# Performance work log

Measured on AMD Instinct MI355X. Metric: run time of the kernel, lower is better.

Reference implementation:

```python
import jax, jax.numpy as jnp
import numpy as np

# Dimensions (source globals scaled to production: r=256 residues, s=128 sequences)
S, R, CM, CZ, C, H = 128, 256, 256, 128, 32, 8
EPS = 1e-5  # torch LayerNorm default


def setup_inputs() -> dict:
    key = jax.random.key(0)
    ks = jax.random.split(key, 14)
    msa = jax.random.normal(ks[0], (S, R, CM), dtype=jnp.float32)
    pair = jax.random.normal(ks[1], (R, R, CZ), dtype=jnp.float32)
    u = lambda k, shape, fan: jax.random.uniform(k, shape, jnp.float32, -1.0 / np.sqrt(fan), 1.0 / np.sqrt(fan))
    return {
        "msa": msa,
        "pair": pair,
        # per-head LayerNorm affine params (stacked over head axis)
        "ln_msa_g": 1.0 + 0.1 * jax.random.normal(ks[2], (H, CM), dtype=jnp.float32),
        "ln_msa_b": 0.1 * jax.random.normal(ks[3], (H, CM), dtype=jnp.float32),
        "ln_pair_g": 1.0 + 0.1 * jax.random.normal(ks[4], (H, CZ), dtype=jnp.float32),
        "ln_pair_b": 0.1 * jax.random.normal(ks[5], (H, CZ), dtype=jnp.float32),
        # per-head projections (torch Linear without bias; stored as (in, out))
        "Wq": u(ks[6], (H, CM, C), CM),
        "Wk": u(ks[7], (H, CM, C), CM),
        "Wv": u(ks[8], (H, CM, C), CM),
        "Wg": u(ks[9], (H, CM, C), CM),
        "Wb": u(ks[10], (H, CZ, S), CZ),  # linear_b: c_z -> s
        # output projection c*H -> c_m (with bias)
        "Wo": u(ks[11], (H * C, CM), H * C),
        "bo": u(ks[12], (CM,), H * C),
    }


def _forward(msa, pair, ln_msa_g, ln_msa_b, ln_pair_g, ln_pair_b, Wq, Wk, Wv, Wg, Wb, Wo, bo):
    # LayerNorm normalization is head-independent; only affine differs per head.
    mu = msa.mean(-1, keepdims=True)
    var = msa.var(-1, keepdims=True)
    nm = (msa - mu) * jax.lax.rsqrt(var + EPS)              # (S, R, CM)
    p = nm[None] * ln_msa_g[:, None, None, :] + ln_msa_b[:, None, None, :]  # (H, S, R, CM)

    q = jnp.einsum("hsrc,hcd->hsrd", p, Wq)                  # (H, S, R, C)
    k = jnp.einsum("hsrc,hcd->hsrd", p, Wk)
    v = jnp.einsum("hsrc,hcd->hsrd", p, Wv)
    g = jax.nn.sigmoid(jnp.einsum("hsrc,hcd->hsrd", p, Wg))

    pmu = pair.mean(-1, keepdims=True)
    pvar = pair.var(-1, keepdims=True)
    npair = (pair - pmu) * jax.lax.rsqrt(pvar + EPS)         # (R, R, CZ)
    pp = npair[None] * ln_pair_g[:, None, None, :] + ln_pair_b[:, None, None, :]  # (H, R, R, CZ)
    bflat = jnp.einsum("hijc,hcs->hijs", pp, Wb)             # (H, R, R, S)
    # Faithful to torch: b = linear_b(flat_pair).view(s, r, r) -- a raw
    # row-major reinterpretation (NOT a transpose).
    b = bflat.reshape(H, S, R, R)

    inv_sqrt_c = np.float32(1.0 / np.sqrt(C))
    scores = (jnp.einsum("hsid,hsjd->hsij", q, k) + b) * inv_sqrt_c  # (H, S, R, R)
    # Source softmax is over dim=-2 (the query/row axis), faithful here.
    a = jax.nn.softmax(scores, axis=-2)
    o = g * jnp.einsum("hsij,hsjd->hsid", a, v)              # (H, S, R, C)

    # concat heads on last dim: (S, R, H*C)
    cat = jnp.transpose(o, (1, 2, 0, 3)).reshape(S, R, H * C)
    return cat @ Wo + bo                                      # (S, R, CM)


def reference(msa, pair, ln_msa_g, ln_msa_b, ln_pair_g, ln_pair_b, Wq, Wk, Wv, Wg, Wb, Wo, bo):
    return _forward(msa, pair, ln_msa_g, ln_msa_b, ln_pair_g, ln_pair_b, Wq, Wk, Wv, Wg, Wb, Wo, bo)
```

## Files before the change

### kernel.cpp

```cpp
#include <hip/hip_runtime.h>
#include <hip/hip_bf16.h>


namespace {
constexpr int S_ = 128, R_ = 256, CM_ = 256, CZ_ = 128, C_ = 32, H_ = 8;
constexpr int SR_ = S_ * R_;
constexpr int RR_ = R_ * R_;
constexpr float EPS_ = 1e-5f;
constexpr float ISC_ = 0.17677669529663687f;

constexpr size_t OFF_WC  = 0;
constexpr size_t OFF_BC  = 131072;
constexpr size_t OFF_BBP = 132096;
constexpr size_t F32_END = 133120;
constexpr size_t BF_BASE = F32_END * 4;
constexpr size_t QKVG_ELEMS  = (size_t)H_ * SR_ * C_;
constexpr size_t CAT_ELEMS   = (size_t)SR_ * CM_;
constexpr size_t WBT_ELEMS   = (size_t)H_ * 128 * 128;
constexpr size_t WOT_ELEMS   = (size_t)256 * 256;
constexpr size_t PAIRN_ELEMS = (size_t)RR_ * 128;
constexpr size_t MSAN_ELEMS  = (size_t)SR_ * 256;
constexpr size_t NEED_BYTES =
    BF_BASE +
    (4 * QKVG_ELEMS + CAT_ELEMS + WBT_ELEMS + WOT_ELEMS + PAIRN_ELEMS + MSAN_ELEMS) * 2;
}

typedef unsigned short bf_t;
typedef short s8v __attribute__((ext_vector_type(8)));
typedef float f4v __attribute__((ext_vector_type(4)));

__device__ __forceinline__ unsigned pk2(float lo, float hi) {
  __hip_bfloat162 t = __float22bfloat162_rn(float2{lo, hi});
  return *reinterpret_cast<unsigned*>(&t);
}
__device__ __forceinline__ bf_t pk1(float v) {
  __hip_bfloat16 t = __float2bfloat16(v);
  return *reinterpret_cast<bf_t*>(&t);
}
__device__ __forceinline__ float uplo(unsigned u) { return __uint_as_float(u << 16); }
__device__ __forceinline__ f4v mfma16(s8v a, s8v b, f4v c) {
  return __builtin_amdgcn_mfma_f32_16x16x32_bf16(a, b, c, 0, 0, 0);
}
__device__ __forceinline__ s8v ld8(const bf_t* p) { return *reinterpret_cast<const s8v*>(p); }

__global__ __launch_bounds__(512) void norm_all_k(const float* __restrict__ pair,
                                                  const float* __restrict__ msa,
                                                  bf_t* __restrict__ pairN,
                                                  bf_t* __restrict__ msaN) {
  int b = blockIdx.x;
  int lane = threadIdx.x & 63;
  if (b < RR_ / 8) {
    int row = b * 8 + (threadIdx.x >> 6);
    float2 v = reinterpret_cast<const float2*>(pair + (size_t)row * CZ_)[lane];
    float s = v.x + v.y;
    float s2 = v.x * v.x + v.y * v.y;
    for (int off = 32; off; off >>= 1) {
      s += __shfl_xor(s, off);
      s2 += __shfl_xor(s2, off);
    }
    float m = s / CZ_;
    float rs = rsqrtf(s2 / CZ_ - m * m + EPS_);
    reinterpret_cast<unsigned*>(pairN)[(size_t)row * 64 + lane] =
        pk2((v.x - m) * rs, (v.y - m) * rs);
  } else {
    int row = (b - RR_ / 8) * 8 + (threadIdx.x >> 6);
    float4 v = reinterpret_cast<const float4*>(msa + (size_t)row * CM_)[lane];
    float s = v.x + v.y + v.z + v.w;
    float s2 = v.x * v.x + v.y * v.y + v.z * v.z + v.w * v.w;
    for (int off = 32; off; off >>= 1) {
      s += __shfl_xor(s, off);
      s2 += __shfl_xor(s2, off);
    }
    float m = s / CM_;
    float rs = rsqrtf(s2 / CM_ - m * m + EPS_);
    uint2 wv;
    wv.x = pk2((v.x - m) * rs, (v.y - m) * rs);
    wv.y = pk2((v.z - m) * rs, (v.w - m) * rs);
    reinterpret_cast<uint2*>(msaN)[(size_t)row * 64 + lane] = wv;
  }
}

__global__ void prep_small_k(const float* __restrict__ lnb_m, const float* __restrict__ lnb_p,
                             const float* __restrict__ Wq, const float* __restrict__ Wk,
                             const float* __restrict__ Wv, const float* __restrict__ Wg,
                             const float* __restrict__ Wb, float* __restrict__ bc,
                             float* __restrict__ bbp) {
  int b = blockIdx.x;
  int t = threadIdx.x;
  if (b < H_) {
    int h = b;
    int m = t >> 5, d = t & 31;
    const float* Wsrc = (m == 0) ? Wq : (m == 1) ? Wk : (m == 2) ? Wv : Wg;
    float scale = (m == 0) ? ISC_ : 1.0f;
    float bias = 0.f;
    for (int c = 0; c < CM_; c++) bias += lnb_m[h * CM_ + c] * Wsrc[((size_t)h * CM_ + c) * C_ + d];
    bc[h * 128 + t] = bias * scale;
  } else {
    int h = b - H_;
    float bias = 0.f;
    for (int c = 0; c < CZ_; c++) bias += lnb_p[h * CZ_ + c] * Wb[((size_t)h * CZ_ + c) * S_ + t];
    bbp[h * 128 + t] = bias * ISC_;
  }
}

__global__ __launch_bounds__(256) void prep_wide_k(
    const float* __restrict__ lng_m, const float* __restrict__ lng_p,
    const float* __restrict__ Wq, const float* __restrict__ Wk, const float* __restrict__ Wv,
    const float* __restrict__ Wg, const float* __restrict__ Wb, const float* __restrict__ Wo,
    bf_t* __restrict__ wct, bf_t* __restrict__ wbt, bf_t* __restrict__ wot) {
  int idx = blockIdx.x * 256 + threadIdx.x;
  if (idx < 262144) {
    int h = idx >> 15, rem = idx & 32767;
    int j = rem >> 8, c = rem & 255;
    int m = j >> 5, d = j & 31;
    const float* Wsrc = (m == 0) ? Wq : (m == 1) ? Wk : (m == 2) ? Wv : Wg;
    float scale = (m == 0) ? ISC_ : 1.0f;
    wct[idx] = pk1(lng_m[h * CM_ + c] * Wsrc[((size_t)h * CM_ + c) * C_ + d] * scale);
  } else if (idx < 262144 + 131072) {
    int i2 = idx - 262144;
    int h = i2 >> 14, rem = i2 & 16383;
    int t = rem >> 7, c = rem & 127;
    wbt[i2] = pk1(lng_p[h * CZ_ + c] * Wb[((size_t)h * CZ_ + c) * S_ + t] * ISC_);
  } else {
    int i3 = idx - 262144 - 131072;
    int n = i3 >> 8, k = i3 & 255;
    wot[i3] = pk1(Wo[(size_t)k * 256 + n]);
  }
}

__global__ __launch_bounds__(512, 1) void qkvg_mfma_k(
    const bf_t* __restrict__ msaN, const bf_t* __restrict__ wct, const float* __restrict__ bc,
    bf_t* __restrict__ q, bf_t* __restrict__ k, bf_t* __restrict__ v, bf_t* __restrict__ g) {
  __shared__ bf_t sm_a[128 * 256];
  __shared__ bf_t sm_w[128 * 256];
  int ib = blockIdx.x;
  int tid = threadIdx.x;
  int w = tid >> 6, l = tid & 63;
  int l15 = l & 15, l4 = l >> 4;
  int iw = w >> 2, jw = w & 3;
  int sr0 = ib * 128;
  int sx7 = l15 & 7;
#pragma unroll
  for (int rep = 0; rep < 8; rep++) {
    int flat = rep * 512 + tid;
    int row = flat >> 5, c = flat & 31;
    *reinterpret_cast<uint4*>(&sm_a[row * 256 + ((c ^ (row & 7)) << 3)]) =
        *reinterpret_cast<const uint4*>(msaN + (size_t)(sr0 + row) * 256 + c * 8);
  }
  for (int h = 0; h < H_; h++) {
    __syncthreads();
#pragma unroll
    for (int rep = 0; rep < 8; rep++) {
      int flat = rep * 512 + tid;
      int row = flat >> 5, c = flat & 31;
      *reinterpret_cast<uint4*>(&sm_w[row * 256 + ((c ^ (row & 7)) << 3)]) =
          *reinterpret_cast<const uint4*>(wct + ((size_t)h * 128 + row) * 256 + c * 8);
    }
    f4v acc[4][2];
#pragma unroll
    for (int jt = 0; jt < 2; jt++) {
      float bb = bc[h * 128 + jw * 32 + jt * 16 + l15];
#pragma unroll
      for (int it = 0; it < 4; it++) acc[it][jt] = f4v{bb, bb, bb, bb};
    }
    __syncthreads();
#pragma unroll
    for (int ks = 0; ks < 8; ks++) {
      int ch = ks * 4 + l4;
      s8v a[4], b[2];
#pragma unroll
      for (int it = 0; it < 4; it++)
        a[it] = ld8(&sm_a[(iw * 64 + it * 16 + l15) * 256 + ((ch ^ sx7) << 3)]);
#pragma unroll
      for (int jt = 0; jt < 2; jt++)
        b[jt] = ld8(&sm_w[(jw * 32 + jt * 16 + l15) * 256 + ((ch ^ sx7) << 3)]);
#pragma unroll
      for (int it = 0; it < 4; it++)
#pragma unroll
        for (int jt = 0; jt < 2; jt++) acc[it][jt] = mfma16(a[it], b[jt], acc[it][jt]);
    }
#pragma unroll
    for (int it = 0; it < 4; it++) {
#pragma unroll
      for (int jt = 0; jt < 2; jt++) {
        int j = jw * 32 + jt * 16 + l15;
        int m_ = j >> 5, d = j & 31;
        bf_t* dst = (m_ == 0) ? q : (m_ == 1) ? k : (m_ == 2) ? v : g;
#pragma unroll
        for (int r = 0; r < 4; r++) {
          int i = iw * 64 + it * 16 + l4 * 4 + r;
          float val = acc[it][jt][r];
          if (m_ == 3) val = 1.f / (1.f + __expf(-val));
          dst[((size_t)h * SR_ + sr0 + i) * C_ + d] = pk1(val);
        }
      }
    }
  }
}

__global__ __launch_bounds__(512, 1) void attn_mfma_k(
    const bf_t* __restrict__ pairN, const bf_t* __restrict__ wbt,
    const float* __restrict__ bbp, const bf_t* __restrict__ qg, const bf_t* __restrict__ kg,
    const bf_t* __restrict__ vg, const bf_t* __restrict__ gg, bf_t* __restrict__ cat) {
  __shared__ bf_t sm_pN[256 * 128];
  __shared__ bf_t sm_wt[64 * 128];
  __shared__ bf_t sm_p[256 * 64];
  __shared__ bf_t sm_q[256 * 40];
  __shared__ bf_t sm_k[64 * 40];
  __shared__ bf_t sm_vt[32 * 64];
  __shared__ float sm_redm[4 * 64];
  __shared__ float sm_reds[4 * 64];

  int b = blockIdx.x;
  int x = b & 7, t = b >> 3;
  int round = t >> 5, inner = t & 31;
  int sl = inner >> 3, h = inner & 7;
  int s = (round * 8 + x) * 4 + sl;

  int tid = threadIdx.x;
  int w = tid >> 6, l = tid & 63;
  int l15 = l & 15, l4 = l >> 4;
  int iw = w >> 1, jw = w & 1;
  int iw2 = w >> 1, dw = w & 1;
  size_t base = ((size_t)h * SR_ + (size_t)s * R_) * C_;

#pragma unroll
  for (int rep = 0; rep < 2; rep++) {
    int flat = rep * 512 + tid;
    int row = flat >> 2, c = flat & 3;
    *reinterpret_cast<uint4*>(&sm_q[row * 40 + c * 8]) =
        *reinterpret_cast<const uint4*>(qg + base + (size_t)row * C_ + c * 8);
  }

  f4v accO[4];
#pragma unroll
  for (int it = 0; it < 4; it++) accO[it] = f4v{0.f, 0.f, 0.f, 0.f};

  for (int p = 0; p < 2; p++) {
    __syncthreads();
#pragma unroll
    for (int rep = 0; rep < 8; rep++) {
      int flat = rep * 512 + tid;
      int row = flat >> 4, c = flat & 15;
      int gr = (2 * s + (row >> 7)) * 256 + 2 * (row & 127) + p;
      *reinterpret_cast<uint4*>(&sm_pN[row * 128 + ((c ^ (row & 7)) << 3)]) =
          *reinterpret_cast<const uint4*>(pairN + (size_t)gr * 128 + c * 8);
    }
    for (int jh = 0; jh < 2; jh++) {
      int j0 = p * 128 + jh * 64;
      __syncthreads();
#pragma unroll
      for (int rep = 0; rep < 2; rep++) {
        int flat = rep * 512 + tid;
        int row = flat >> 4, c = flat & 15;
        *reinterpret_cast<uint4*>(&sm_wt[row * 128 + ((c ^ (row & 7)) << 3)]) =
            *reinterpret_cast<const uint4*>(wbt + ((size_t)h * 128 + jh * 64 + row) * 128 +
                                            c * 8);
      }
      if (tid < 256) {
        int row = tid >> 2, c = tid & 3;
        *reinterpret_cast<uint4*>(&sm_k[row * 40 + c * 8]) =
            *reinterpret_cast<const uint4*>(kg + base + (size_t)(j0 + row) * C_ + c * 8);
      } else {
        int t2 = tid - 256;
        int j = t2 >> 2, dc = t2 & 3;
        uint4 u = *reinterpret_cast<const uint4*>(vg + base + (size_t)(j0 + j) * C_ + dc * 8);
        unsigned uu[4] = {u.x, u.y, u.z, u.w};
#pragma unroll
        for (int e = 0; e < 8; e++) {
          int d = dc * 8 + e;
          bf_t val = (bf_t)((uu[e >> 1] >> ((e & 1) * 16)) & 0xffff);
          sm_vt[d * 64 + ((((j >> 3) ^ (d & 7)) << 3) + (j & 7))] = val;
        }
      }
      f4v acc[4][2];
      {
        float bb0 = bbp[h * 128 + jh * 64 + jw * 32 + l15];
        float bb1 = bbp[h * 128 + jh * 64 + jw * 32 + 16 + l15];
#pragma unroll
        for (int it = 0; it < 4; it++) {
          acc[it][0] = f4v{bb0, bb0, bb0, bb0};
          acc[it][1] = f4v{bb1, bb1, bb1, bb1};
        }
      }
      __syncthreads();
      int sx7 = l15 & 7;
#pragma unroll
      for (int ks = 0; ks < 4; ks++) {
        int ch = (ks * 4 + l4);
        s8v a[4], b2[2];
#pragma unroll
        for (int it = 0; it < 4; it++)
          a[it] = ld8(&sm_pN[(iw * 64 + it * 16 + l15) * 128 + ((ch ^ sx7) << 3)]);
#pragma unroll
        for (int u = 0; u < 2; u++)
          b2[u] = ld8(&sm_wt[(jw * 32 + u * 16 + l15) * 128 + ((ch ^ sx7) << 3)]);
#pragma unroll
        for (int it = 0; it < 4; it++) {
          acc[it][0] = mfma16(a[it], b2[0], acc[it][0]);
          acc[it][1] = mfma16(a[it], b2[1], acc[it][1]);
        }
      }
      {
        s8v qa[4], kb[2];
#pragma unroll
        for (int it = 0; it < 4; it++)
          qa[it] = ld8(&sm_q[(iw * 64 + it * 16 + l15) * 40 + l4 * 8]);
#pragma unroll
        for (int u = 0; u < 2; u++)
          kb[u] = ld8(&sm_k[(jw * 32 + u * 16 + l15) * 40 + l4 * 8]);
#pragma unroll
        for (int it = 0; it < 4; it++) {
          acc[it][0] = mfma16(qa[it], kb[0], acc[it][0]);
          acc[it][1] = mfma16(qa[it], kb[1], acc[it][1]);
        }
      }
      float fac[2], mloc[2];
#pragma unroll
      for (int u = 0; u < 2; u++) {
        float m0 = -1e30f;
#pragma unroll
        for (int it = 0; it < 4; it++)
#pragma unroll
          for (int r = 0; r < 4; r++) m0 = fmaxf(m0, acc[it][u][r]);
        m0 = fmaxf(m0, __shfl_xor(m0, 16));
        m0 = fmaxf(m0, __shfl_xor(m0, 32));
        float s0 = 0.f;
#pragma unroll
        for (int it = 0; it < 4; it++)
#pragma unroll
          for (int r = 0; r < 4; r++) {
            float e = __expf(acc[it][u][r] - m0);
            acc[it][u][r] = e;
            s0 += e;
          }
        s0 += __shfl_xor(s0, 16);
        s0 += __shfl_xor(s0, 32);
        mloc[u] = m0;
        if (l < 16) {
          sm_redm[iw * 64 + jw * 32 + u * 16 + l] = m0;
          sm_reds[iw * 64 + jw * 32 + u * 16 + l] = s0;
        }
      }
      __syncthreads();
#pragma unroll
      for (int u = 0; u < 2; u++) {
        int jc = jw * 32 + u * 16 + l15;
        float M = fmaxf(fmaxf(sm_redm[jc], sm_redm[64 + jc]),
                        fmaxf(sm_redm[128 + jc], sm_redm[192 + jc]));
        float tot = 0.f;
#pragma unroll
        for (int gx = 0; gx < 4; gx++)
          tot += sm_reds[gx * 64 + jc] * __expf(sm_redm[gx * 64 + jc] - M);
        fac[u] = __expf(mloc[u] - M) / tot;
#pragma unroll
        for (int it = 0; it < 4; it++)
#pragma unroll
          for (int r = 0; r < 4; r++) {
            int i = iw * 64 + it * 16 + l4 * 4 + r;
            sm_p[i * 64 + ((((jc >> 3) ^ (i & 7)) << 3) + (jc & 7))] =
                pk1(acc[it][u][r] * fac[u]);
          }
      }
      __syncthreads();
#pragma unroll
      for (int ks = 0; ks < 2; ks++) {
        int ch = ks * 4 + l4;
        s8v vb = ld8(&sm_vt[(dw * 16 + l15) * 64 + ((ch ^ sx7) << 3)]);
#pragma unroll
        for (int it = 0; it < 4; it++) {
          s8v pa = ld8(&sm_p[(iw2 * 64 + it * 16 + l15) * 64 + ((ch ^ sx7) << 3)]);
          accO[it] = mfma16(pa, vb, accO[it]);
        }
      }
    }
  }
#pragma unroll
  for (int it = 0; it < 4; it++) {
#pragma unroll
    for (int r = 0; r < 4; r++) {
      int i = iw2 * 64 + it * 16 + l4 * 4 + r;
      int d = dw * 16 + l15;
      float gf = uplo((unsigned)gg[base + (size_t)i * C_ + d]);
      cat[((size_t)s * R_ + i) * 256 + h * 32 + d] = pk1(accO[it][r] * gf);
    }
  }
}

__global__ __launch_bounds__(512, 1) void out_mfma_k(const bf_t* __restrict__ cat,
                                                     const bf_t* __restrict__ wot,
                                                     const float* __restrict__ bo,
                                                     float* __restrict__ out) {
  __shared__ bf_t sm_a[128 * 256];
  __shared__ bf_t sm_b[128 * 256];
  int ib = blockIdx.x;
  int tid = threadIdx.x;
  int w = tid >> 6, l = tid & 63;
  int l15 = l & 15, l4 = l >> 4, sx7 = l15 & 7;
  int iw = w >> 2, jw = w & 3;
  int sr0 = ib * 128;
#pragma unroll
  for (int rep = 0; rep < 8; rep++) {
    int flat = rep * 512 + tid;
    int row = flat >> 5, c = flat & 31;
    *reinterpret_cast<uint4*>(&sm_a[row * 256 + ((c ^ (row & 7)) << 3)]) =
        *reinterpret_cast<const uint4*>(cat + (size_t)(sr0 + row) * 256 + c * 8);
  }
  for (int nb = 0; nb < 2; nb++) {
    __syncthreads();
#pragma unroll
    for (int rep = 0; rep < 8; rep++) {
      int flat = rep * 512 + tid;
      int row = flat >> 5, c = flat & 31;
      *reinterpret_cast<uint4*>(&sm_b[row * 256 + ((c ^ (row & 7)) << 3)]) =
          *reinterpret_cast<const uint4*>(wot + (size_t)(nb * 128 + row) * 256 + c * 8);
    }
    f4v acc[4][2];
#pragma unroll
    for (int jt = 0; jt < 2; jt++) {
      float bb = bo[nb * 128 + jw * 32 + jt * 16 + l15];
#pragma unroll
      for (int it = 0; it < 4; it++) acc[it][jt] = f4v{bb, bb, bb, bb};
    }
    __syncthreads();
#pragma unroll
    for (int ks = 0; ks < 8; ks++) {
      int ch = ks * 4 + l4;
      s8v a[4], b[2];
#pragma unroll
      for (int it = 0; it < 4; it++)
        a[it] = ld8(&sm_a[(iw * 64 + it * 16 + l15) * 256 + ((ch ^ sx7) << 3)]);
#pragma unroll
      for (int jt = 0; jt < 2; jt++)
        b[jt] = ld8(&sm_b[(jw * 32 + jt * 16 + l15) * 256 + ((ch ^ sx7) << 3)]);
#pragma unroll
      for (int it = 0; it < 4; it++)
#pragma unroll
        for (int jt = 0; jt < 2; jt++) acc[it][jt] = mfma16(a[it], b[jt], acc[it][jt]);
    }
#pragma unroll
    for (int it = 0; it < 4; it++)
#pragma unroll
      for (int jt = 0; jt < 2; jt++) {
        int n = nb * 128 + jw * 32 + jt * 16 + l15;
#pragma unroll
        for (int r = 0; r < 4; r++) {
          int i = iw * 64 + it * 16 + l4 * 4 + r;
          out[(size_t)(sr0 + i) * 256 + n] = acc[it][jt][r];
        }
      }
  }
}

extern "C" void kernel_launch(void* const* d_in, const int* in_sizes, int n_in, void* d_out,
                              int out_size, void* d_ws, size_t ws_size, hipStream_t stream) {
  if (ws_size < NEED_BYTES) return;

  const float* msa = (const float*)d_in[0];
  const float* pair = (const float*)d_in[1];
  const float* lng_m = (const float*)d_in[2];
  const float* lnb_m = (const float*)d_in[3];
  const float* lng_p = (const float*)d_in[4];
  const float* lnb_p = (const float*)d_in[5];
  const float* Wq = (const float*)d_in[6];
  const float* Wk = (const float*)d_in[7];
  const float* Wv = (const float*)d_in[8];
  const float* Wg = (const float*)d_in[9];
  const float* Wb = (const float*)d_in[10];
  const float* Wo = (const float*)d_in[11];
  const float* bo = (const float*)d_in[12];
  float* out = (float*)d_out;
  float* ws = (float*)d_ws;

  bf_t* wct = (bf_t*)(ws + OFF_WC);
  float* bc = ws + OFF_BC;
  float* bbp = ws + OFF_BBP;
  bf_t* qb = (bf_t*)((char*)d_ws + BF_BASE);
  bf_t* kb = qb + QKVG_ELEMS;
  bf_t* vb = kb + QKVG_ELEMS;
  bf_t* gb = vb + QKVG_ELEMS;
  bf_t* cat = gb + QKVG_ELEMS;
  bf_t* wbt = cat + CAT_ELEMS;
  bf_t* wot = wbt + WBT_ELEMS;
  bf_t* pairN = wot + WOT_ELEMS;
  bf_t* msaN = pairN + PAIRN_ELEMS;

  norm_all_k<<<RR_ / 8 + SR_ / 8, 512, 0, stream>>>(pair, msa, pairN, msaN);
  prep_small_k<<<2 * H_, 128, 0, stream>>>(lnb_m, lnb_p, Wq, Wk, Wv, Wg, Wb, bc, bbp);
  prep_wide_k<<<1792, 256, 0, stream>>>(lng_m, lng_p, Wq, Wk, Wv, Wg, Wb, Wo, wct, wbt, wot);
  qkvg_mfma_k<<<SR_ / 128, 512, 0, stream>>>(msaN, wct, bc, qb, kb, vb, gb);
  attn_mfma_k<<<S_ * H_, 512, 0, stream>>>(pairN, wbt, bbp, qb, kb, vb, gb, cat);
  out_mfma_k<<<SR_ / 128, 512, 0, stream>>>(cat, wot, bo, out);
}
```

Before: 168.1 us.

## Merge prep kernels into one launch and load Q/K fragments directly to registers

Fuses the three preprocessing kernels (normalization, bias folding, weight conversion) into a single launch, removing two kernel launches and their gaps. In the attention kernel, Q fragments are loaded once straight from global memory into registers and K fragments per tile are loaded directly too, dropping the sm_q/sm_k shared buffers and their staging stores. The wbt tile load moves to the first 256 threads, and the other half builds the transposed V. This cuts LDS traffic and footprint but relies on uncoalesced-ish direct global fragment loads and unbalances the loading work across threads.

```diff
diff --git a/kernel.cpp b/kernel.cpp
--- a/kernel.cpp
+++ b/kernel.cpp
@@ -43,14 +43,20 @@
 }
 __device__ __forceinline__ s8v ld8(const bf_t* p) { return *reinterpret_cast<const s8v*>(p); }
 
-__global__ __launch_bounds__(512) void norm_all_k(const float* __restrict__ pair,
-                                                  const float* __restrict__ msa,
-                                                  bf_t* __restrict__ pairN,
-                                                  bf_t* __restrict__ msaN) {
+__global__ __launch_bounds__(512) void prep_all_k(
+    const float* __restrict__ pair, const float* __restrict__ msa,
+    const float* __restrict__ lng_m, const float* __restrict__ lnb_m,
+    const float* __restrict__ lng_p, const float* __restrict__ lnb_p,
+    const float* __restrict__ Wq, const float* __restrict__ Wk, const float* __restrict__ Wv,
+    const float* __restrict__ Wg, const float* __restrict__ Wb, const float* __restrict__ Wo,
+    bf_t* __restrict__ pairN, bf_t* __restrict__ msaN, bf_t* __restrict__ wct,
+    bf_t* __restrict__ wbt, bf_t* __restrict__ wot, float* __restrict__ bc,
+    float* __restrict__ bbp) {
   int b = blockIdx.x;
-  int lane = threadIdx.x & 63;
-  if (b < RR_ / 8) {
-    int row = b * 8 + (threadIdx.x >> 6);
+  int tid = threadIdx.x;
+  int lane = tid & 63;
+  if (b < 8192) {
+    int row = b * 8 + (tid >> 6);
     float2 v = reinterpret_cast<const float2*>(pair + (size_t)row * CZ_)[lane];
     float s = v.x + v.y;
     float s2 = v.x * v.x + v.y * v.y;
@@ -62,8 +68,8 @@
     float rs = rsqrtf(s2 / CZ_ - m * m + EPS_);
     reinterpret_cast<unsigned*>(pairN)[(size_t)row * 64 + lane] =
         pk2((v.x - m) * rs, (v.y - m) * rs);
-  } else {
-    int row = (b - RR_ / 8) * 8 + (threadIdx.x >> 6);
+  } else if (b < 12288) {
+    int row = (b - 8192) * 8 + (tid >> 6);
     float4 v = reinterpret_cast<const float4*>(msa + (size_t)row * CM_)[lane];
     float s = v.x + v.y + v.z + v.w;
     float s2 = v.x * v.x + v.y * v.y + v.z * v.z + v.w * v.w;
@@ -77,54 +83,44 @@
     wv.x = pk2((v.x - m) * rs, (v.y - m) * rs);
     wv.y = pk2((v.z - m) * rs, (v.w - m) * rs);
     reinterpret_cast<uint2*>(msaN)[(size_t)row * 64 + lane] = wv;
-  }
-}
-
-__global__ void prep_small_k(const float* __restrict__ lnb_m, const float* __restrict__ lnb_p,
-                             const float* __restrict__ Wq, const float* __restrict__ Wk,
-                             const float* __restrict__ Wv, const float* __restrict__ Wg,
-                             const float* __restrict__ Wb, float* __restrict__ bc,
-                             float* __restrict__ bbp) {
-  int b = blockIdx.x;
-  int t = threadIdx.x;
-  if (b < H_) {
-    int h = b;
-    int m = t >> 5, d = t & 31;
-    const float* Wsrc = (m == 0) ? Wq : (m == 1) ? Wk : (m == 2) ? Wv : Wg;
-    float scale = (m == 0) ? ISC_ : 1.0f;
-    float bias = 0.f;
-    for (int c = 0; c < CM_; c++) bias += lnb_m[h * CM_ + c] * Wsrc[((size_t)h * CM_ + c) * C_ + d];
-    bc[h * 128 + t] = bias * scale;
+  } else if (b < 13184) {
+    int idx = (b - 12288) * 512 + tid;
+    if (idx < 262144) {
+      int h = idx >> 15, rem = idx & 32767;
+      int j = rem >> 8, c = rem & 255;
+      int m = j >> 5, d = j & 31;
+      const float* Wsrc = (m == 0) ? Wq : (m == 1) ? Wk : (m == 2) ? Wv : Wg;
+      float scale = (m == 0) ? ISC_ : 1.0f;
+      wct[idx] = pk1(lng_m[h * CM_ + c] * Wsrc[((size_t)h * CM_ + c) * C_ + d] * scale);
+    } else if (idx < 262144 + 131072) {
+      int i2 = idx - 262144;
+      int h = i2 >> 14, rem = i2 & 16383;
+      int t = rem >> 7, c = rem & 127;
+      wbt[i2] = pk1(lng_p[h * CZ_ + c] * Wb[((size_t)h * CZ_ + c) * S_ + t] * ISC_);
+    } else {
+      int i3 = idx - 262144 - 131072;
+      int n = i3 >> 8, k = i3 & 255;
+      wot[i3] = pk1(Wo[(size_t)k * 256 + n]);
+    }
   } else {
-    int h = b - H_;
-    float bias = 0.f;
-    for (int c = 0; c < CZ_; c++) bias += lnb_p[h * CZ_ + c] * Wb[((size_t)h * CZ_ + c) * S_ + t];
-    bbp[h * 128 + t] = bias * ISC_;
-  }
-}
-
-__global__ __launch_bounds__(256) void prep_wide_k(
-    const float* __restrict__ lng_m, const float* __restrict__ lng_p,
-    const float* __restrict__ Wq, const float* __restrict__ Wk, const float* __restrict__ Wv,
-    const float* __restrict__ Wg, const float* __restrict__ Wb, const float* __restrict__ Wo,
-    bf_t* __restrict__ wct, bf_t* __restrict__ wbt, bf_t* __restrict__ wot) {
-  int idx = blockIdx.x * 256 + threadIdx.x;
-  if (idx < 262144) {
-    int h = idx >> 15, rem = idx & 32767;
-    int j = rem >> 8, c = rem & 255;
-    int m = j >> 5, d = j & 31;
-    const float* Wsrc = (m == 0) ? Wq : (m == 1) ? Wk : (m == 2) ? Wv : Wg;
-    float scale = (m == 0) ? ISC_ : 1.0f;
-    wct[idx] = pk1(lng_m[h * CM_ + c] * Wsrc[((size_t)h * CM_ + c) * C_ + d] * scale);
-  } else if (idx < 262144 + 131072) {
-    int i2 = idx - 262144;
-    int h = i2 >> 14, rem = i2 & 16383;
-    int t = rem >> 7, c = rem & 127;
-    wbt[i2] = pk1(lng_p[h * CZ_ + c] * Wb[((size_t)h * CZ_ + c) * S_ + t] * ISC_);
-  } else {
-    int i3 = idx - 262144 - 131072;
-    int n = i3 >> 8, k = i3 & 255;
-    wot[i3] = pk1(Wo[(size_t)k * 256 + n]);
+    int ob = (b - 13184) * 4 + (tid >> 7);
+    int t = tid & 127;
+    if (ob < H_) {
+      int h = ob;
+      int m = t >> 5, d = t & 31;
+      const float* Wsrc = (m == 0) ? Wq : (m == 1) ? Wk : (m == 2) ? Wv : Wg;
+      float scale = (m == 0) ? ISC_ : 1.0f;
+      float bias = 0.f;
+      for (int c = 0; c < CM_; c++)
+        bias += lnb_m[h * CM_ + c] * Wsrc[((size_t)h * CM_ + c) * C_ + d];
+      bc[h * 128 + t] = bias * scale;
+    } else {
+      int h = ob - H_;
+      float bias = 0.f;
+      for (int c = 0; c < CZ_; c++)
+        bias += lnb_p[h * CZ_ + c] * Wb[((size_t)h * CZ_ + c) * S_ + t];
+      bbp[h * 128 + t] = bias * ISC_;
+    }
   }
 }
 
@@ -205,8 +201,6 @@
   __shared__ bf_t sm_pN[256 * 128];
   __shared__ bf_t sm_wt[64 * 128];
   __shared__ bf_t sm_p[256 * 64];
-  __shared__ bf_t sm_q[256 * 40];
-  __shared__ bf_t sm_k[64 * 40];
   __shared__ bf_t sm_vt[32 * 64];
   __shared__ float sm_redm[4 * 64];
   __shared__ float sm_reds[4 * 64];
@@ -222,15 +216,13 @@
   int l15 = l & 15, l4 = l >> 4;
   int iw = w >> 1, jw = w & 1;
   int iw2 = w >> 1, dw = w & 1;
+  int sx7 = l15 & 7;
   size_t base = ((size_t)h * SR_ + (size_t)s * R_) * C_;
 
-#pragma unroll
-  for (int rep = 0; rep < 2; rep++) {
-    int flat = rep * 512 + tid;
-    int row = flat >> 2, c = flat & 3;
-    *reinterpret_cast<uint4*>(&sm_q[row * 40 + c * 8]) =
-        *reinterpret_cast<const uint4*>(qg + base + (size_t)row * C_ + c * 8);
-  }
+  s8v qa[4];
+#pragma unroll
+  for (int it = 0; it < 4; it++)
+    qa[it] = ld8(&qg[base + (size_t)(iw * 64 + it * 16 + l15) * C_ + l4 * 8]);
 
   f4v accO[4];
 #pragma unroll
@@ -248,19 +240,18 @@
     }
     for (int jh = 0; jh < 2; jh++) {
       int j0 = p * 128 + jh * 64;
+      s8v kb0 = ld8(&kg[base + (size_t)(j0 + jw * 32 + l15) * C_ + l4 * 8]);
+      s8v kb1 = ld8(&kg[base + (size_t)(j0 + jw * 32 + 16 + l15) * C_ + l4 * 8]);
       __syncthreads();
-#pragma unroll
-      for (int rep = 0; rep < 2; rep++) {
-        int flat = rep * 512 + tid;
-        int row = flat >> 4, c = flat & 15;
-        *reinterpret_cast<uint4*>(&sm_wt[row * 128 + ((c ^ (row & 7)) << 3)]) =
-            *reinterpret_cast<const uint4*>(wbt + ((size_t)h * 128 + jh * 64 + row) * 128 +
-                                            c * 8);
-      }
       if (tid < 256) {
-        int row = tid >> 2, c = tid & 3;
-        *reinterpret_cast<uint4*>(&sm_k[row * 40 + c * 8]) =
-            *reinterpret_cast<const uint4*>(kg + base + (size_t)(j0 + row) * C_ + c * 8);
+#pragma unroll
+        for (int rep = 0; rep < 4; rep++) {
+          int flat = rep * 256 + tid;
+          int row = flat >> 4, c = flat & 15;
+          *reinterpret_cast<uint4*>(&sm_wt[row * 128 + ((c ^ (row & 7)) << 3)]) =
+              *reinterpret_cast<const uint4*>(wbt + ((size_t)h * 128 + jh * 64 + row) * 128 +
+                                              c * 8);
+        }
       } else {
         int t2 = tid - 256;
         int j = t2 >> 2, dc = t2 & 3;
@@ -284,7 +275,6 @@
         }
       }
       __syncthreads();
-      int sx7 = l15 & 7;
 #pragma unroll
       for (int ks = 0; ks < 4; ks++) {
         int ch = (ks * 4 + l4);
@@ -301,19 +291,10 @@
           acc[it][1] = mfma16(a[it], b2[1], acc[it][1]);
         }
       }
-      {
-        s8v qa[4], kb[2];
-#pragma unroll
-        for (int it = 0; it < 4; it++)
-          qa[it] = ld8(&sm_q[(iw * 64 + it * 16 + l15) * 40 + l4 * 8]);
-#pragma unroll
-        for (int u = 0; u < 2; u++)
-          kb[u] = ld8(&sm_k[(jw * 32 + u * 16 + l15) * 40 + l4 * 8]);
-#pragma unroll
-        for (int it = 0; it < 4; it++) {
-          acc[it][0] = mfma16(qa[it], kb[0], acc[it][0]);
-          acc[it][1] = mfma16(qa[it], kb[1], acc[it][1]);
-        }
+#pragma unroll
+      for (int it = 0; it < 4; it++) {
+        acc[it][0] = mfma16(qa[it], kb0, acc[it][0]);
+        acc[it][1] = mfma16(qa[it], kb1, acc[it][1]);
       }
       float fac[2], mloc[2];
 #pragma unroll
@@ -485,9 +466,8 @@
   bf_t* pairN = wot + WOT_ELEMS;
   bf_t* msaN = pairN + PAIRN_ELEMS;
 
-  norm_all_k<<<RR_ / 8 + SR_ / 8, 512, 0, stream>>>(pair, msa, pairN, msaN);
-  prep_small_k<<<2 * H_, 128, 0, stream>>>(lnb_m, lnb_p, Wq, Wk, Wv, Wg, Wb, bc, bbp);
-  prep_wide_k<<<1792, 256, 0, stream>>>(lng_m, lng_p, Wq, Wk, Wv, Wg, Wb, Wo, wct, wbt, wot);
+  prep_all_k<<<13188, 512, 0, stream>>>(pair, msa, lng_m, lnb_m, lng_p, lnb_p, Wq, Wk, Wv, Wg,
+                                        Wb, Wo, pairN, msaN, wct, wbt, wot, bc, bbp);
   qkvg_mfma_k<<<SR_ / 128, 512, 0, stream>>>(msaN, wct, bc, qb, kb, vb, gb);
   attn_mfma_k<<<S_ * H_, 512, 0, stream>>>(pairN, wbt, bbp, qb, kb, vb, gb, cat);
   out_mfma_k<<<SR_ / 128, 512, 0, stream>>>(cat, wot, bo, out);
```

Result: faster. 159.5 us (-5.1%).
